# Performance work log

Hardware: AMD Instinct MI355X
Metric: run time of the kernel (lower is better)

## Reference

```python
import jax, jax.numpy as jnp
import numpy as np

TK, HA = 3, 8          # num_blocks, num_heads
AVGF = 32              # num_submatrices
LN_EPS = 1e-5


def _layernorm(x, g, b):
    m = jnp.mean(x, axis=-1, keepdims=True)
    v = jnp.mean((x - m) ** 2, axis=-1, keepdims=True)
    return (x - m) / jnp.sqrt(v + LN_EPS) * g + b


def setup_inputs() -> dict:
    key = jax.random.key(0)
    ks = jax.random.split(key, 12)
    A, B, T = 16, 128, 512
    M = A * B              # 2048
    Dh = M // HA           # 256
    H = 4 * M              # 8192
    s = 0.05               # scale randn params so activations stay finite
    return {
        "x": jax.random.normal(ks[0], (A, B, T), jnp.float32),
        "weight": jax.random.normal(ks[1], (M, M), jnp.float32) * s,
        "Wq": jax.random.normal(ks[2], (TK, HA, Dh, M), jnp.float32) * s,
        "Wk": jax.random.normal(ks[3], (TK, HA, Dh, M), jnp.float32) * s,
        "Wv": jax.random.normal(ks[4], (TK, HA, Dh, M), jnp.float32) * s,
        "Wo": jax.random.normal(ks[5], (TK, M, M), jnp.float32) * s,
        "ln1_g": jnp.ones((M,), jnp.float32),
        "ln1_b": jnp.zeros((M,), jnp.float32),
        "ln2_g": jnp.ones((M,), jnp.float32),
        "ln2_b": jnp.zeros((M,), jnp.float32),
        "fc1_w": jax.random.normal(ks[6], (H, M), jnp.float32) * 0.02,
        "fc1_b": jnp.zeros((H,), jnp.float32),
        "fc2_w": jax.random.normal(ks[7], (M, H), jnp.float32) * 0.02,
        "fc2_b": jnp.zeros((M,), jnp.float32),
    }


def reference(x, weight, Wq, Wk, Wv, Wo, ln1_g, ln1_b, ln2_g, ln2_b,
              fc1_w, fc1_b, fc2_w, fc2_b):
    A, B, T = x.shape
    M = A * B
    Dh = M // HA
    seg = T // AVGF
    # redefine(): transpose(0,2) -> (T,B,A), segment-average along time, flatten
    xt = jnp.transpose(x, (2, 1, 0))                       # (T, B, A)
    xc = xt.reshape(AVGF, seg, B, A).mean(axis=1)          # (AVGF, B, A)
    xcf = xc.reshape(AVGF, M)                              # (AVGF, M)
    # savespace[i] = weight @ x[i]  + sinusoidal positional bias
    pos = jnp.arange(AVGF, dtype=jnp.float32)[:, None]
    je = jnp.arange(0, M, 2, dtype=jnp.float32)
    ang = pos / (10000.0 ** (2.0 * je / M))                # (AVGF, M/2)
    bias = jnp.zeros((AVGF, M), jnp.float32)
    bias = bias.at[:, 0::2].set(jnp.sin(ang)).at[:, 1::2].set(jnp.cos(ang))
    s0 = xcf @ weight.T + bias                             # (AVGF, M)
    scale = 1.0 / jnp.sqrt(jnp.float32(Dh))

    # Sequential recurrence over tokens: vcum[a] carries the cumulative
    # softmax-weighted V sum (softmax over a scalar == 1) per block/head.
    def step(vcum, s):
        for a in range(TK):
            xn = _layernorm(s, ln1_g, ln1_b)
            q = jnp.einsum('hdm,m->hd', Wq[a], xn)         # (HA, Dh)
            k = jnp.einsum('hdm,m->hd', Wk[a], xn)
            v = jnp.einsum('hdm,m->hd', Wv[a], xn)
            scores = jnp.sum(q * k, axis=-1) * scale       # (HA,) scalars
            w = jax.nn.softmax(scores[:, None], axis=-1)[:, 0]  # ones
            vcum = vcum.at[a].add(w[:, None] * v)
            s = Wo[a] @ vcum[a].reshape(-1) + s
            s = _layernorm(s, ln2_g, ln2_b) + s
            h = jax.nn.gelu(fc1_w @ s + fc1_b, approximate=False)
            s = fc2_w @ h + fc2_b
        return vcum, s

    vcum0 = jnp.zeros((TK, HA, Dh), s0.dtype)
    _, out = jax.lax.scan(step, vcum0, s0)                 # (AVGF, M)
    return out.reshape(AVGF, B, A)
```

## Files before the change

kernel.cpp:

```cpp
#include <hip/hip_runtime.h>
#include <hip/hip_bf16.h>
#include <math.h>

typedef __attribute__((ext_vector_type(8))) short short8;
typedef __attribute__((ext_vector_type(4))) float floatx4;

__device__ inline unsigned f2bf1(float f) {
    union { float f; unsigned u; } v; v.f = f;
    return (v.u + 0x8000u) >> 16;
}

__device__ inline short8 pack8(float4 a, float4 b) {
    short8 r;
    r[0] = (short)f2bf1(a.x); r[1] = (short)f2bf1(a.y);
    r[2] = (short)f2bf1(a.z); r[3] = (short)f2bf1(a.w);
    r[4] = (short)f2bf1(b.x); r[5] = (short)f2bf1(b.y);
    r[6] = (short)f2bf1(b.z); r[7] = (short)f2bf1(b.w);
    return r;
}

__global__ __launch_bounds__(128) void avg_k(const float* __restrict__ x,
                                             float* __restrict__ xcf) {
    int blk = blockIdx.x;
    int a = blk >> 7, b = blk & 127;
    int t = threadIdx.x;
    const float4 v = *(const float4*)(x + ((size_t)a * 128 + b) * 512 + t * 4);
    float s = v.x + v.y + v.z + v.w;
    s += __shfl_xor(s, 1);
    s += __shfl_xor(s, 2);
    if ((t & 3) == 0) {
        int seg = t >> 2;
        xcf[seg * 2048 + b * 16 + a] = s * (1.0f / 16.0f);
    }
}

__global__ __launch_bounds__(256) void ln_k(const float* __restrict__ Sin,
                                            const float* __restrict__ g,
                                            const float* __restrict__ b,
                                            float* __restrict__ out, int addres) {
    __shared__ float red[8];
    const int row = blockIdx.x, t = threadIdx.x;
    const float* xr = Sin + (size_t)row * 2048;
    float4 v0 = *(const float4*)(xr + t * 4);
    float4 v1 = *(const float4*)(xr + 1024 + t * 4);
    float s = v0.x + v0.y + v0.z + v0.w + v1.x + v1.y + v1.z + v1.w;
    for (int o = 32; o; o >>= 1) s += __shfl_down(s, o);
    if ((t & 63) == 0) red[t >> 6] = s;
    __syncthreads();
    float mean = (red[0] + red[1] + red[2] + red[3]) * (1.0f / 2048.0f);
    float d0 = v0.x - mean, d1 = v0.y - mean, d2 = v0.z - mean, d3 = v0.w - mean;
    float e0 = v1.x - mean, e1 = v1.y - mean, e2 = v1.z - mean, e3 = v1.w - mean;
    float s2 = d0*d0 + d1*d1 + d2*d2 + d3*d3 + e0*e0 + e1*e1 + e2*e2 + e3*e3;
    for (int o = 32; o; o >>= 1) s2 += __shfl_down(s2, o);
    if ((t & 63) == 0) red[4 + (t >> 6)] = s2;
    __syncthreads();
    float var = (red[4] + red[5] + red[6] + red[7]) * (1.0f / 2048.0f);
    float rs = 1.0f / sqrtf(var + 1e-5f);
    float4 g0 = *(const float4*)(g + t * 4);
    float4 g1 = *(const float4*)(g + 1024 + t * 4);
    float4 b0 = *(const float4*)(b + t * 4);
    float4 b1 = *(const float4*)(b + 1024 + t * 4);
    float4 o0, o1;
    o0.x = d0 * rs * g0.x + b0.x; o0.y = d1 * rs * g0.y + b0.y;
    o0.z = d2 * rs * g0.z + b0.z; o0.w = d3 * rs * g0.w + b0.w;
    o1.x = e0 * rs * g1.x + b1.x; o1.y = e1 * rs * g1.y + b1.y;
    o1.z = e2 * rs * g1.z + b1.z; o1.w = e3 * rs * g1.w + b1.w;
    if (addres) {
        o0.x += v0.x; o0.y += v0.y; o0.z += v0.z; o0.w += v0.w;
        o1.x += v1.x; o1.y += v1.y; o1.z += v1.z; o1.w += v1.w;
    }
    *(float4*)(out + (size_t)row * 2048 + t * 4) = o0;
    *(float4*)(out + (size_t)row * 2048 + 1024 + t * 4) = o1;
}

__global__ __launch_bounds__(256) void cumsum_k(float* __restrict__ V) {
    int c = blockIdx.x * 256 + threadIdx.x;
    float run = 0.f;
#pragma unroll
    for (int i = 0; i < 32; i++) { run += V[i * 2048 + c]; V[i * 2048 + c] = run; }
}

__global__ __launch_bounds__(256) void gelu_k(float* __restrict__ H,
                                              const float* __restrict__ b1) {
    int idx4 = blockIdx.x * 256 + threadIdx.x;
    int col4 = idx4 & 2047;
    float4 v = *(const float4*)(H + (size_t)idx4 * 4);
    const float4 bb = *(const float4*)(b1 + col4 * 4);
    v.x += bb.x; v.y += bb.y; v.z += bb.z; v.w += bb.w;
    v.x = 0.5f * v.x * (1.0f + erff(v.x * 0.70710678118654752f));
    v.y = 0.5f * v.y * (1.0f + erff(v.y * 0.70710678118654752f));
    v.z = 0.5f * v.z * (1.0f + erff(v.z * 0.70710678118654752f));
    v.w = 0.5f * v.w * (1.0f + erff(v.w * 0.70710678118654752f));
    *(float4*)(H + (size_t)idx4 * 4) = v;
}

template<int KCHUNK, int MODE>
__global__ __launch_bounds__(256) void gemm_k(const float* __restrict__ X,
                                              const float* __restrict__ W,
                                              float* __restrict__ C,
                                              const float* __restrict__ bias,
                                              int N, int K) {
    constexpr int PITCH = KCHUNK + 8;
    __shared__ unsigned short Xs[32 * PITCH];
    const int tid = threadIdx.x;
    const int bx = blockIdx.x, by = blockIdx.y;
    const int kb0 = by * KCHUNK;

    constexpr int NF4 = 32 * (KCHUNK / 4);
    for (int f = tid; f < NF4; f += 256) {
        int row = f / (KCHUNK / 4), c4 = f % (KCHUNK / 4);
        const float4 v = *(const float4*)(X + (size_t)row * K + kb0 + c4 * 4);
        ushort4 p;
        p.x = (unsigned short)f2bf1(v.x);
        p.y = (unsigned short)f2bf1(v.y);
        p.z = (unsigned short)f2bf1(v.z);
        p.w = (unsigned short)f2bf1(v.w);
        *(ushort4*)&Xs[row * PITCH + c4 * 4] = p;
    }
    __syncthreads();

    const int w = tid >> 6, lane = tid & 63;
    const int q = lane >> 4, r16 = lane & 15;
    const int nb = bx * 128 + w * 32;
    floatx4 acc[2][2] = {};
    const float* wp0 = W + (size_t)(nb + r16) * K + kb0 + q * 8;
    const float* wp1 = W + (size_t)(nb + 16 + r16) * K + kb0 + q * 8;

#pragma unroll
    for (int kk = 0; kk < KCHUNK; kk += 32) {
        short8 a0 = *(const short8*)&Xs[r16 * PITCH + kk + q * 8];
        short8 a1 = *(const short8*)&Xs[(16 + r16) * PITCH + kk + q * 8];
        {
            float4 u0 = *(const float4*)(wp0 + kk);
            float4 u1 = *(const float4*)(wp0 + kk + 4);
            short8 bf = pack8(u0, u1);
            acc[0][0] = __builtin_amdgcn_mfma_f32_16x16x32_bf16(a0, bf, acc[0][0], 0, 0, 0);
            acc[1][0] = __builtin_amdgcn_mfma_f32_16x16x32_bf16(a1, bf, acc[1][0], 0, 0, 0);
        }
        {
            float4 u0 = *(const float4*)(wp1 + kk);
            float4 u1 = *(const float4*)(wp1 + kk + 4);
            short8 bf = pack8(u0, u1);
            acc[0][1] = __builtin_amdgcn_mfma_f32_16x16x32_bf16(a0, bf, acc[0][1], 0, 0, 0);
            acc[1][1] = __builtin_amdgcn_mfma_f32_16x16x32_bf16(a1, bf, acc[1][1], 0, 0, 0);
        }
    }

#pragma unroll
    for (int mt = 0; mt < 2; mt++)
#pragma unroll
        for (int nt = 0; nt < 2; nt++)
#pragma unroll
            for (int e = 0; e < 4; e++) {
                int i = mt * 16 + q * 4 + e;
                int n = nb + nt * 16 + r16;
                float v = acc[mt][nt][e];
                if (MODE == 1 && by == 0) v += bias[n];
                if (MODE == 2 && by == 0) {
                    int ne = n & ~1;
                    float ang = (float)i * __expf(-(float)ne * (9.210340371976184f / 1024.0f));
                    v += (n & 1) ? cosf(ang) : sinf(ang);
                }
                atomicAdd(C + (size_t)i * N + n, v);
            }
}

extern "C" void kernel_launch(void* const* d_in, const int* in_sizes, int n_in,
                              void* d_out, int out_size, void* d_ws, size_t ws_size,
                              hipStream_t stream) {
    const float* x      = (const float*)d_in[0];
    const float* weight = (const float*)d_in[1];
    const float* Wv     = (const float*)d_in[4];
    const float* Wo     = (const float*)d_in[5];
    const float* ln1g   = (const float*)d_in[6];
    const float* ln1b   = (const float*)d_in[7];
    const float* ln2g   = (const float*)d_in[8];
    const float* ln2b   = (const float*)d_in[9];
    const float* fc1w   = (const float*)d_in[10];
    const float* fc1b   = (const float*)d_in[11];
    const float* fc2w   = (const float*)d_in[12];
    const float* fc2b   = (const float*)d_in[13];
    float* ws  = (float*)d_ws;
    float* xcf = ws;
    float* S   = ws + 65536;
    float* Xn  = ws + 131072;
    float* V   = ws + 196608;
    float* H   = ws + 262144;
    float* out = (float*)d_out;

    avg_k<<<2048, 128, 0, stream>>>(x, xcf);

    hipMemsetAsync(S, 0, 65536 * 4, stream);
    gemm_k<128, 2><<<dim3(16, 16), 256, 0, stream>>>(xcf, weight, S, nullptr, 2048, 2048);

    for (int a = 0; a < 3; a++) {
        ln_k<<<32, 256, 0, stream>>>(S, ln1g, ln1b, Xn, 0);
        hipMemsetAsync(V, 0, 65536 * 4, stream);
        gemm_k<128, 0><<<dim3(16, 16), 256, 0, stream>>>(Xn, Wv + (size_t)a * 4194304, V, nullptr, 2048, 2048);
        cumsum_k<<<8, 256, 0, stream>>>(V);
        gemm_k<128, 0><<<dim3(16, 16), 256, 0, stream>>>(V, Wo + (size_t)a * 4194304, S, nullptr, 2048, 2048);
        ln_k<<<32, 256, 0, stream>>>(S, ln2g, ln2b, S, 1);
        hipMemsetAsync(H, 0, 262144 * 4, stream);
        gemm_k<256, 0><<<dim3(64, 8), 256, 0, stream>>>(S, fc1w, H, nullptr, 8192, 2048);
        gelu_k<<<256, 256, 0, stream>>>(H, fc1b);
        float* Co = (a == 2) ? out : S;
        hipMemsetAsync(Co, 0, 65536 * 4, stream);
        gemm_k<256, 1><<<dim3(16, 32), 256, 0, stream>>>(H, fc2w, Co, fc2b, 2048, 8192);
    }
}
```

Measured before the change: 497.2 us.

## Fuse layernorm, cumsum and GELU into GEMM prologues and halve N tiles

Standalone layernorm, cumsum and GELU kernels are removed. Their work moves into the X-staging prologue of the following GEMM: a small stats kernel supplies the per-row mean and rstd, and each GEMM applies the normalisation, residual add, running cumsum or bias+GELU while converting to bf16. This cuts kernel launches and full-tensor round-trips through global memory. Each block now computes one 16-column N tile per wave instead of two, which doubles the grid for more parallelism over the weight streams. In exchange, the fused elementwise work, especially the erf, is recomputed redundantly by every column block.

```diff
diff --git a/kernel.cpp b/kernel.cpp
--- a/kernel.cpp
+++ b/kernel.cpp
@@ -1,5 +1,4 @@
 #include <hip/hip_runtime.h>
-#include <hip/hip_bf16.h>
 #include <math.h>
 
 typedef __attribute__((ext_vector_type(8))) short short8;
@@ -17,6 +16,10 @@
     r[4] = (short)f2bf1(b.x); r[5] = (short)f2bf1(b.y);
     r[6] = (short)f2bf1(b.z); r[7] = (short)f2bf1(b.w);
     return r;
+}
+
+__device__ inline float gelu1(float x) {
+    return 0.5f * x * (1.0f + erff(x * 0.70710678118654752f));
 }
 
 __global__ __launch_bounds__(128) void avg_k(const float* __restrict__ x,
@@ -34,10 +37,8 @@
     }
 }
 
-__global__ __launch_bounds__(256) void ln_k(const float* __restrict__ Sin,
-                                            const float* __restrict__ g,
-                                            const float* __restrict__ b,
-                                            float* __restrict__ out, int addres) {
+__global__ __launch_bounds__(256) void stats_k(const float* __restrict__ Sin,
+                                               float* __restrict__ st) {
     __shared__ float red[8];
     const int row = blockIdx.x, t = threadIdx.x;
     const float* xr = Sin + (size_t)row * 2048;
@@ -54,51 +55,21 @@
     for (int o = 32; o; o >>= 1) s2 += __shfl_down(s2, o);
     if ((t & 63) == 0) red[4 + (t >> 6)] = s2;
     __syncthreads();
-    float var = (red[4] + red[5] + red[6] + red[7]) * (1.0f / 2048.0f);
-    float rs = 1.0f / sqrtf(var + 1e-5f);
-    float4 g0 = *(const float4*)(g + t * 4);
-    float4 g1 = *(const float4*)(g + 1024 + t * 4);
-    float4 b0 = *(const float4*)(b + t * 4);
-    float4 b1 = *(const float4*)(b + 1024 + t * 4);
-    float4 o0, o1;
-    o0.x = d0 * rs * g0.x + b0.x; o0.y = d1 * rs * g0.y + b0.y;
-    o0.z = d2 * rs * g0.z + b0.z; o0.w = d3 * rs * g0.w + b0.w;
-    o1.x = e0 * rs * g1.x + b1.x; o1.y = e1 * rs * g1.y + b1.y;
-    o1.z = e2 * rs * g1.z + b1.z; o1.w = e3 * rs * g1.w + b1.w;
-    if (addres) {
-        o0.x += v0.x; o0.y += v0.y; o0.z += v0.z; o0.w += v0.w;
-        o1.x += v1.x; o1.y += v1.y; o1.z += v1.z; o1.w += v1.w;
-    }
-    *(float4*)(out + (size_t)row * 2048 + t * 4) = o0;
-    *(float4*)(out + (size_t)row * 2048 + 1024 + t * 4) = o1;
-}
-
-__global__ __launch_bounds__(256) void cumsum_k(float* __restrict__ V) {
-    int c = blockIdx.x * 256 + threadIdx.x;
-    float run = 0.f;
-#pragma unroll
-    for (int i = 0; i < 32; i++) { run += V[i * 2048 + c]; V[i * 2048 + c] = run; }
-}
-
-__global__ __launch_bounds__(256) void gelu_k(float* __restrict__ H,
-                                              const float* __restrict__ b1) {
-    int idx4 = blockIdx.x * 256 + threadIdx.x;
-    int col4 = idx4 & 2047;
-    float4 v = *(const float4*)(H + (size_t)idx4 * 4);
-    const float4 bb = *(const float4*)(b1 + col4 * 4);
-    v.x += bb.x; v.y += bb.y; v.z += bb.z; v.w += bb.w;
-    v.x = 0.5f * v.x * (1.0f + erff(v.x * 0.70710678118654752f));
-    v.y = 0.5f * v.y * (1.0f + erff(v.y * 0.70710678118654752f));
-    v.z = 0.5f * v.z * (1.0f + erff(v.z * 0.70710678118654752f));
-    v.w = 0.5f * v.w * (1.0f + erff(v.w * 0.70710678118654752f));
-    *(float4*)(H + (size_t)idx4 * 4) = v;
-}
-
-template<int KCHUNK, int MODE>
+    if (t == 0) {
+        float var = (red[4] + red[5] + red[6] + red[7]) * (1.0f / 2048.0f);
+        st[row * 2]     = mean;
+        st[row * 2 + 1] = 1.0f / sqrtf(var + 1e-5f);
+    }
+}
+
+template<int KCHUNK, int NT, int STAGE, int EPI>
 __global__ __launch_bounds__(256) void gemm_k(const float* __restrict__ X,
                                               const float* __restrict__ W,
                                               float* __restrict__ C,
-                                              const float* __restrict__ bias,
+                                              const float* __restrict__ ebias,
+                                              const float* __restrict__ stats,
+                                              const float* __restrict__ sg,
+                                              const float* __restrict__ sb,
                                               int N, int K) {
     constexpr int PITCH = KCHUNK + 8;
     __shared__ unsigned short Xs[32 * PITCH];
@@ -106,23 +77,57 @@
     const int bx = blockIdx.x, by = blockIdx.y;
     const int kb0 = by * KCHUNK;
 
-    constexpr int NF4 = 32 * (KCHUNK / 4);
-    for (int f = tid; f < NF4; f += 256) {
-        int row = f / (KCHUNK / 4), c4 = f % (KCHUNK / 4);
-        const float4 v = *(const float4*)(X + (size_t)row * K + kb0 + c4 * 4);
-        ushort4 p;
-        p.x = (unsigned short)f2bf1(v.x);
-        p.y = (unsigned short)f2bf1(v.y);
-        p.z = (unsigned short)f2bf1(v.z);
-        p.w = (unsigned short)f2bf1(v.w);
-        *(ushort4*)&Xs[row * PITCH + c4 * 4] = p;
+    if constexpr (STAGE == 2) {
+        for (int c = tid; c < KCHUNK; c += 256) {
+            const float* vp = X + kb0 + c;
+            float run = 0.f;
+#pragma unroll
+            for (int r = 0; r < 32; r++) {
+                run += vp[(size_t)r * K];
+                Xs[r * PITCH + c] = (unsigned short)f2bf1(run);
+            }
+        }
+    } else {
+        constexpr int NF4 = 32 * (KCHUNK / 4);
+        for (int f = tid; f < NF4; f += 256) {
+            const int row = f / (KCHUNK / 4), c4 = f % (KCHUNK / 4);
+            const int k0 = kb0 + c4 * 4;
+            float4 v = *(const float4*)(X + (size_t)row * K + k0);
+            if constexpr (STAGE == 1 || STAGE == 11) {
+                const float m = stats[row * 2], rs = stats[row * 2 + 1];
+                const float4 gg = *(const float4*)(sg + k0);
+                const float4 bb = *(const float4*)(sb + k0);
+                float4 o;
+                o.x = (v.x - m) * rs * gg.x + bb.x;
+                o.y = (v.y - m) * rs * gg.y + bb.y;
+                o.z = (v.z - m) * rs * gg.z + bb.z;
+                o.w = (v.w - m) * rs * gg.w + bb.w;
+                if constexpr (STAGE == 11) {
+                    o.x += v.x; o.y += v.y; o.z += v.z; o.w += v.w;
+                }
+                v = o;
+            }
+            if constexpr (STAGE == 3) {
+                const float4 bb = *(const float4*)(sg + k0);
+                v.x = gelu1(v.x + bb.x);
+                v.y = gelu1(v.y + bb.y);
+                v.z = gelu1(v.z + bb.z);
+                v.w = gelu1(v.w + bb.w);
+            }
+            ushort4 p;
+            p.x = (unsigned short)f2bf1(v.x);
+            p.y = (unsigned short)f2bf1(v.y);
+            p.z = (unsigned short)f2bf1(v.z);
+            p.w = (unsigned short)f2bf1(v.w);
+            *(ushort4*)&Xs[row * PITCH + c4 * 4] = p;
+        }
     }
     __syncthreads();
 
     const int w = tid >> 6, lane = tid & 63;
     const int q = lane >> 4, r16 = lane & 15;
-    const int nb = bx * 128 + w * 32;
-    floatx4 acc[2][2] = {};
+    const int nb = bx * (NT * 64) + w * (NT * 16);
+    floatx4 acc[2][NT] = {};
     const float* wp0 = W + (size_t)(nb + r16) * K + kb0 + q * 8;
     const float* wp1 = W + (size_t)(nb + 16 + r16) * K + kb0 + q * 8;
 
@@ -137,7 +142,7 @@
             acc[0][0] = __builtin_amdgcn_mfma_f32_16x16x32_bf16(a0, bf, acc[0][0], 0, 0, 0);
             acc[1][0] = __builtin_amdgcn_mfma_f32_16x16x32_bf16(a1, bf, acc[1][0], 0, 0, 0);
         }
-        {
+        if constexpr (NT == 2) {
             float4 u0 = *(const float4*)(wp1 + kk);
             float4 u1 = *(const float4*)(wp1 + kk + 4);
             short8 bf = pack8(u0, u1);
@@ -149,14 +154,14 @@
 #pragma unroll
     for (int mt = 0; mt < 2; mt++)
 #pragma unroll
-        for (int nt = 0; nt < 2; nt++)
+        for (int nt = 0; nt < NT; nt++)
 #pragma unroll
             for (int e = 0; e < 4; e++) {
                 int i = mt * 16 + q * 4 + e;
                 int n = nb + nt * 16 + r16;
                 float v = acc[mt][nt][e];
-                if (MODE == 1 && by == 0) v += bias[n];
-                if (MODE == 2 && by == 0) {
+                if (EPI == 1 && by == 0) v += ebias[n];
+                if (EPI == 2 && by == 0) {
                     int ne = n & ~1;
                     float ang = (float)i * __expf(-(float)ne * (9.210340371976184f / 1024.0f));
                     v += (n & 1) ? cosf(ang) : sinf(ang);
@@ -183,28 +188,32 @@
     float* ws  = (float*)d_ws;
     float* xcf = ws;
     float* S   = ws + 65536;
-    float* Xn  = ws + 131072;
-    float* V   = ws + 196608;
-    float* H   = ws + 262144;
+    float* V   = ws + 131072;
+    float* H   = ws + 196608;
+    float* st1 = ws + 458752;
+    float* st2 = ws + 458816;
     float* out = (float*)d_out;
 
     avg_k<<<2048, 128, 0, stream>>>(x, xcf);
 
     hipMemsetAsync(S, 0, 65536 * 4, stream);
-    gemm_k<128, 2><<<dim3(16, 16), 256, 0, stream>>>(xcf, weight, S, nullptr, 2048, 2048);
+    gemm_k<128, 1, 0, 2><<<dim3(32, 16), 256, 0, stream>>>(
+        xcf, weight, S, nullptr, nullptr, nullptr, nullptr, 2048, 2048);
 
     for (int a = 0; a < 3; a++) {
-        ln_k<<<32, 256, 0, stream>>>(S, ln1g, ln1b, Xn, 0);
+        stats_k<<<32, 256, 0, stream>>>(S, st1);
         hipMemsetAsync(V, 0, 65536 * 4, stream);
-        gemm_k<128, 0><<<dim3(16, 16), 256, 0, stream>>>(Xn, Wv + (size_t)a * 4194304, V, nullptr, 2048, 2048);
-        cumsum_k<<<8, 256, 0, stream>>>(V);
-        gemm_k<128, 0><<<dim3(16, 16), 256, 0, stream>>>(V, Wo + (size_t)a * 4194304, S, nullptr, 2048, 2048);
-        ln_k<<<32, 256, 0, stream>>>(S, ln2g, ln2b, S, 1);
+        gemm_k<128, 1, 1, 0><<<dim3(32, 16), 256, 0, stream>>>(
+            S, Wv + (size_t)a * 4194304, V, nullptr, st1, ln1g, ln1b, 2048, 2048);
+        gemm_k<128, 1, 2, 0><<<dim3(32, 16), 256, 0, stream>>>(
+            V, Wo + (size_t)a * 4194304, S, nullptr, nullptr, nullptr, nullptr, 2048, 2048);
+        stats_k<<<32, 256, 0, stream>>>(S, st2);
         hipMemsetAsync(H, 0, 262144 * 4, stream);
-        gemm_k<256, 0><<<dim3(64, 8), 256, 0, stream>>>(S, fc1w, H, nullptr, 8192, 2048);
-        gelu_k<<<256, 256, 0, stream>>>(H, fc1b);
+        gemm_k<256, 1, 11, 0><<<dim3(128, 8), 256, 0, stream>>>(
+            S, fc1w, H, nullptr, st2, ln2g, ln2b, 8192, 2048);
         float* Co = (a == 2) ? out : S;
         hipMemsetAsync(Co, 0, 65536 * 4, stream);
-        gemm_k<256, 1><<<dim3(16, 32), 256, 0, stream>>>(H, fc2w, Co, fc2b, 2048, 8192);
-    }
-}
+        gemm_k<256, 1, 3, 1><<<dim3(32, 32), 256, 0, stream>>>(
+            H, fc2w, Co, fc2b, nullptr, fc1b, nullptr, 2048, 8192);
+    }
+}
```

Result: faster. 458.6 us (-7.8%).
